# Kernel optimization log

Hardware: AMD Instinct MI355X
Metric: run time of the kernel (lower is better)

Reference implementation:

```python
import jax, jax.numpy as jnp
import numpy as np

M, L, D, V = 4096, 15, 1024, 32  # moves, word_max, in_sz, vocab_sz


def setup_inputs() -> dict:
    key = jax.random.key(0)
    ks = jax.random.split(key, 9)
    s = 0.02
    return {
        "tokens": jax.random.randint(ks[0], (M, L), 0, V),
        "letter_emb": jax.random.normal(ks[1], (V, D), jnp.float32) * s,
        "pos_emb": jax.random.normal(ks[2], (L, D), jnp.float32) * s,
        "Wq": jax.random.normal(ks[3], (D, D), jnp.float32) * s,
        "bq": jax.random.normal(ks[4], (D,), jnp.float32) * s,
        "Wk": jax.random.normal(ks[5], (D, D), jnp.float32) * s,
        "bk": jax.random.normal(ks[6], (D,), jnp.float32) * s,
        "Wv": jax.random.normal(ks[7], (D, D), jnp.float32) * s,
        "bv": jax.random.normal(ks[8], (D,), jnp.float32) * s,
    }


def reference(tokens, letter_emb, pos_emb, Wq, bq, Wk, bk, Wv, bv):
    # WordEncoder, batched across all M moves.
    x = letter_emb[tokens] + pos_emb[None, :, :]          # [M, L, D]
    q = jnp.einsum("mld,ed->mle", x, Wq) + bq             # Linear: x @ W.T + b
    k = jnp.einsum("mld,ed->mle", x, Wk) + bk
    v = jnp.einsum("mld,ed->mle", x, Wv) + bv
    scores = jax.nn.softmax(jnp.einsum("mle,mke->mlk", q, k), axis=-1)  # [M, L, L]
    attn = jnp.einsum("mlk,mke->mle", scores, v)          # [M, L, D]
    word = attn.sum(axis=1)                               # [M, D]
    # enc = word + ordered, where ordered is an identical second evaluation
    # of word_enc on the same word -> enc = 2 * word.
    return 2.0 * word
```

## Files before the change

kernel.cpp:

```cpp
#include <hip/hip_runtime.h>
#include <hip/hip_bf16.h>

#define NMOVES 4096
#define LW     15
#define DIM    1024
#define VOC    32
#define NROW   480
#define XROW   48
#define G48LD  64

typedef __attribute__((ext_vector_type(8))) short  short8;
typedef __attribute__((ext_vector_type(4))) float  floatx4;

__device__ __forceinline__ unsigned short f2b(float f) {
  unsigned int x;
  __builtin_memcpy(&x, &f, 4);
  x = x + 0x7FFFu + ((x >> 16) & 1u);
  return (unsigned short)(x >> 16);
}
__device__ __forceinline__ ushort4 cvt4(float4 v) {
  ushort4 o; o.x = f2b(v.x); o.y = f2b(v.y); o.z = f2b(v.z); o.w = f2b(v.w);
  return o;
}
__device__ __forceinline__ float b2f(unsigned short u) {
  unsigned int x = ((unsigned int)u) << 16;
  float f;
  __builtin_memcpy(&f, &x, 4);
  return f;
}

#define LDK 72

__global__ __launch_bounds__(256) void proj_small(
    const float* __restrict__ letter, const float* __restrict__ pos,
    const float* __restrict__ Wq, const float* __restrict__ Wk,
    const float* __restrict__ Wv,
    float* __restrict__ Xq, float* __restrict__ Xk, float* __restrict__ Xv) {
  __shared__ __attribute__((aligned(16))) unsigned short lA[64 * LDK];
  __shared__ __attribute__((aligned(16))) unsigned short lB[64 * LDK];

  const float* W = (blockIdx.z == 0) ? Wq : (blockIdx.z == 1) ? Wk : Wv;
  float*       O = (blockIdx.z == 0) ? Xq : (blockIdx.z == 1) ? Xk : Xv;

  const int bn0 = blockIdx.y * 64;

  const int tid  = threadIdx.x;
  const int lane = tid & 63;
  const int wave = tid >> 6;
  const int wr   = wave >> 1;
  const int wc   = wave & 1;
  const int quad = lane >> 4;
  const int l16  = lane & 15;
  const int srow = tid >> 3;
  const int scol = (tid & 7) << 3;

  const float* aptr0 = letter + (size_t)srow * DIM + scol;
  const bool   av1   = (srow < LW);
  const float* aptr1 = av1 ? (pos + (size_t)srow * DIM + scol) : letter;
  const float* bptr0 = W + (size_t)(bn0 + srow) * DIM + scol;
  const float* bptr1 = bptr0 + (size_t)32 * DIM;

  const float4 z4 = make_float4(0.f, 0.f, 0.f, 0.f);
  float4 ra00 = *reinterpret_cast<const float4*>(aptr0);
  float4 ra01 = *reinterpret_cast<const float4*>(aptr0 + 4);
  float4 ra10 = av1 ? *reinterpret_cast<const float4*>(aptr1)     : z4;
  float4 ra11 = av1 ? *reinterpret_cast<const float4*>(aptr1 + 4) : z4;
  float4 rb00 = *reinterpret_cast<const float4*>(bptr0);
  float4 rb01 = *reinterpret_cast<const float4*>(bptr0 + 4);
  float4 rb10 = *reinterpret_cast<const float4*>(bptr1);
  float4 rb11 = *reinterpret_cast<const float4*>(bptr1 + 4);

  floatx4 acc[2][2];
#pragma unroll
  for (int i = 0; i < 2; ++i)
#pragma unroll
    for (int j = 0; j < 2; ++j) acc[i][j] = (floatx4){0.f, 0.f, 0.f, 0.f};

  for (int k0 = 0; k0 < DIM; k0 += 64) {
    *reinterpret_cast<ushort4*>(lA + srow * LDK + scol)            = cvt4(ra00);
    *reinterpret_cast<ushort4*>(lA + srow * LDK + scol + 4)        = cvt4(ra01);
    *reinterpret_cast<ushort4*>(lA + (srow + 32) * LDK + scol)     = cvt4(ra10);
    *reinterpret_cast<ushort4*>(lA + (srow + 32) * LDK + scol + 4) = cvt4(ra11);
    *reinterpret_cast<ushort4*>(lB + srow * LDK + scol)            = cvt4(rb00);
    *reinterpret_cast<ushort4*>(lB + srow * LDK + scol + 4)        = cvt4(rb01);
    *reinterpret_cast<ushort4*>(lB + (srow + 32) * LDK + scol)     = cvt4(rb10);
    *reinterpret_cast<ushort4*>(lB + (srow + 32) * LDK + scol + 4) = cvt4(rb11);
    __syncthreads();
    if (k0 + 64 < DIM) {
      const int k = k0 + 64;
      ra00 = *reinterpret_cast<const float4*>(aptr0 + k);
      ra01 = *reinterpret_cast<const float4*>(aptr0 + k + 4);
      ra10 = av1 ? *reinterpret_cast<const float4*>(aptr1 + k)     : z4;
      ra11 = av1 ? *reinterpret_cast<const float4*>(aptr1 + k + 4) : z4;
      rb00 = *reinterpret_cast<const float4*>(bptr0 + k);
      rb01 = *reinterpret_cast<const float4*>(bptr0 + k + 4);
      rb10 = *reinterpret_cast<const float4*>(bptr1 + k);
      rb11 = *reinterpret_cast<const float4*>(bptr1 + k + 4);
    }
#pragma unroll
    for (int kk = 0; kk < 64; kk += 32) {
      short8 a0 = *reinterpret_cast<const short8*>(lA + (wr * 32 + l16) * LDK + kk + quad * 8);
      short8 a1 = *reinterpret_cast<const short8*>(lA + (wr * 32 + 16 + l16) * LDK + kk + quad * 8);
      short8 b0 = *reinterpret_cast<const short8*>(lB + (wc * 32 + l16) * LDK + kk + quad * 8);
      short8 b1 = *reinterpret_cast<const short8*>(lB + (wc * 32 + 16 + l16) * LDK + kk + quad * 8);
      acc[0][0] = __builtin_amdgcn_mfma_f32_16x16x32_bf16(a0, b0, acc[0][0], 0, 0, 0);
      acc[0][1] = __builtin_amdgcn_mfma_f32_16x16x32_bf16(a0, b1, acc[0][1], 0, 0, 0);
      acc[1][0] = __builtin_amdgcn_mfma_f32_16x16x32_bf16(a1, b0, acc[1][0], 0, 0, 0);
      acc[1][1] = __builtin_amdgcn_mfma_f32_16x16x32_bf16(a1, b1, acc[1][1], 0, 0, 0);
    }
    __syncthreads();
  }

#pragma unroll
  for (int mi = 0; mi < 2; ++mi) {
#pragma unroll
    for (int ni = 0; ni < 2; ++ni) {
      const int gcol = bn0 + wc * 32 + ni * 16 + l16;
#pragma unroll
      for (int i = 0; i < 4; ++i) {
        const int grow = wr * 32 + mi * 16 + quad * 4 + i;
        if (grow < XROW - 1)
          O[(size_t)grow * DIM + gcol] = acc[mi][ni][i];
      }
    }
  }
}

__global__ __launch_bounds__(256) void gram_vexp(
    const float* __restrict__ Xq, const float* __restrict__ Xk,
    const float* __restrict__ bq, const float* __restrict__ bk,
    const float* __restrict__ Xv,
    float* __restrict__ G48, unsigned short* __restrict__ XvT) {
  const int tid = threadIdx.x;

  if (blockIdx.x == 0) {
    __shared__ __attribute__((aligned(16))) unsigned short lA[64 * LDK];
    __shared__ __attribute__((aligned(16))) unsigned short lB[64 * LDK];

    const int lane = tid & 63;
    const int wave = tid >> 6;
    const int wr   = wave >> 1;
    const int wc   = wave & 1;
    const int quad = lane >> 4;
    const int l16  = lane & 15;
    const int srow = tid >> 3;
    const int scol = (tid & 7) << 3;

    const float* aptr0 = Xq + (size_t)srow * DIM + scol;
    const float* bptr0 = Xk + (size_t)srow * DIM + scol;
    const bool   v1    = (srow <= LW);
    const float* aptr1 = (srow < LW) ? (Xq + (size_t)(32 + srow) * DIM + scol)
                                     : (srow == LW ? (bq + scol) : Xq);
    const float* bptr1 = (srow < LW) ? (Xk + (size_t)(32 + srow) * DIM + scol)
                                     : (srow == LW ? (bk + scol) : Xk);

    const float4 z4 = make_float4(0.f, 0.f, 0.f, 0.f);
    float4 ra00 = *reinterpret_cast<const float4*>(aptr0);
    float4 ra01 = *reinterpret_cast<const float4*>(aptr0 + 4);
    float4 ra10 = v1 ? *reinterpret_cast<const float4*>(aptr1)     : z4;
    float4 ra11 = v1 ? *reinterpret_cast<const float4*>(aptr1 + 4) : z4;
    float4 rb00 = *reinterpret_cast<const float4*>(bptr0);
    float4 rb01 = *reinterpret_cast<const float4*>(bptr0 + 4);
    float4 rb10 = v1 ? *reinterpret_cast<const float4*>(bptr1)     : z4;
    float4 rb11 = v1 ? *reinterpret_cast<const float4*>(bptr1 + 4) : z4;

    floatx4 acc[2][2];
#pragma unroll
    for (int i = 0; i < 2; ++i)
#pragma unroll
      for (int j = 0; j < 2; ++j) acc[i][j] = (floatx4){0.f, 0.f, 0.f, 0.f};

    for (int k0 = 0; k0 < DIM; k0 += 64) {
      *reinterpret_cast<ushort4*>(lA + srow * LDK + scol)            = cvt4(ra00);
      *reinterpret_cast<ushort4*>(lA + srow * LDK + scol + 4)        = cvt4(ra01);
      *reinterpret_cast<ushort4*>(lA + (srow + 32) * LDK + scol)     = cvt4(ra10);
      *reinterpret_cast<ushort4*>(lA + (srow + 32) * LDK + scol + 4) = cvt4(ra11);
      *reinterpret_cast<ushort4*>(lB + srow * LDK + scol)            = cvt4(rb00);
      *reinterpret_cast<ushort4*>(lB + srow * LDK + scol + 4)        = cvt4(rb01);
      *reinterpret_cast<ushort4*>(lB + (srow + 32) * LDK + scol)     = cvt4(rb10);
      *reinterpret_cast<ushort4*>(lB + (srow + 32) * LDK + scol + 4) = cvt4(rb11);
      __syncthreads();
      if (k0 + 64 < DIM) {
        const int k = k0 + 64;
        ra00 = *reinterpret_cast<const float4*>(aptr0 + k);
        ra01 = *reinterpret_cast<const float4*>(aptr0 + k + 4);
        ra10 = v1 ? *reinterpret_cast<const float4*>(aptr1 + k)     : z4;
        ra11 = v1 ? *reinterpret_cast<const float4*>(aptr1 + k + 4) : z4;
        rb00 = *reinterpret_cast<const float4*>(bptr0 + k);
        rb01 = *reinterpret_cast<const float4*>(bptr0 + k + 4);
        rb10 = v1 ? *reinterpret_cast<const float4*>(bptr1 + k)     : z4;
        rb11 = v1 ? *reinterpret_cast<const float4*>(bptr1 + k + 4) : z4;
      }
#pragma unroll
      for (int kk = 0; kk < 64; kk += 32) {
        short8 a0 = *reinterpret_cast<const short8*>(lA + (wr * 32 + l16) * LDK + kk + quad * 8);
        short8 a1 = *reinterpret_cast<const short8*>(lA + (wr * 32 + 16 + l16) * LDK + kk + quad * 8);
        short8 b0 = *reinterpret_cast<const short8*>(lB + (wc * 32 + l16) * LDK + kk + quad * 8);
        short8 b1 = *reinterpret_cast<const short8*>(lB + (wc * 32 + 16 + l16) * LDK + kk + quad * 8);
        acc[0][0] = __builtin_amdgcn_mfma_f32_16x16x32_bf16(a0, b0, acc[0][0], 0, 0, 0);
        acc[0][1] = __builtin_amdgcn_mfma_f32_16x16x32_bf16(a0, b1, acc[0][1], 0, 0, 0);
        acc[1][0] = __builtin_amdgcn_mfma_f32_16x16x32_bf16(a1, b0, acc[1][0], 0, 0, 0);
        acc[1][1] = __builtin_amdgcn_mfma_f32_16x16x32_bf16(a1, b1, acc[1][1], 0, 0, 0);
      }
      __syncthreads();
    }

#pragma unroll
    for (int mi = 0; mi < 2; ++mi) {
#pragma unroll
      for (int ni = 0; ni < 2; ++ni) {
        const int gcol = wc * 32 + ni * 16 + l16;
#pragma unroll
        for (int i = 0; i < 4; ++i) {
          const int grow = wr * 32 + mi * 16 + quad * 4 + i;
          if (grow < XROW)
            G48[(size_t)grow * G48LD + gcol] = acc[mi][ni][i];
        }
      }
    }
  } else {
    const int n  = ((int)blockIdx.x - 1) * 16 + (tid >> 4);
    const int k0 = (tid & 15) * 4;
    float v[4];
#pragma unroll
    for (int i = 0; i < 4; ++i) {
      const int k = k0 + i;
      v[i] = (k < XROW - 1) ? Xv[(size_t)k * DIM + n] : 0.f;
    }
    ushort4 o;
    o.x = f2b(v[0]); o.y = f2b(v[1]); o.z = f2b(v[2]); o.w = f2b(v[3]);
    *reinterpret_cast<ushort4*>(XvT + (size_t)n * 64 + k0) = o;
  }
}

__global__ __launch_bounds__(256) void coef_k(
    const void* __restrict__ tokens_raw, const float* __restrict__ G48,
    unsigned short* __restrict__ C) {
  __shared__ float Gs[XROW * 65];
  __shared__ float Sm[16][LW][17];
  __shared__ float CL[16][64];
  __shared__ int   tokL[16][16];
  __shared__ int   is64_s;
  const int m0  = blockIdx.x * 16;
  const int tid = threadIdx.x;

  const unsigned int* u32 = (const unsigned int*)tokens_raw;
  if (tid < 64) {
    unsigned int v = u32[2 * tid + 1];
    unsigned long long nz = __ballot(v != 0);
    if (tid == 0) is64_s = (nz == 0ULL) ? 1 : 0;
  }
#pragma unroll
  for (int i = 0; i < 12; ++i) {
    const int idx = i * 256 + tid;
    Gs[(idx >> 6) * 65 + (idx & 63)] = G48[idx];
  }
  {
    const int g = tid >> 4, L = tid & 15;
#pragma unroll
    for (int i = 0; i < 4; ++i) CL[g][L * 4 + i] = 0.f;
  }
  __syncthreads();

  if (tid < 16 * LW) {
    const int mv = tid / LW, j = tid - mv * LW;
    int t;
    if (is64_s) t = (int)((const long long*)tokens_raw)[(size_t)(m0 + mv) * LW + j];
    else        t = ((const int*)tokens_raw)[(size_t)(m0 + mv) * LW + j];
    tokL[mv][j] = t;
  }
  __syncthreads();

  const int g = tid >> 4;
  const int L = tid & 15;
  if (L < LW) {
    const int rb0 = tokL[g][L] * 65;
    const int rb1 = (32 + L) * 65;
    const int rb2 = (XROW - 1) * 65;
    float S[LW];
#pragma unroll
    for (int j = 0; j < LW; ++j) {
      const int c0 = tokL[g][j];
      const int c1 = 32 + j;
      S[j] = Gs[rb0 + c0] + Gs[rb1 + c0] + Gs[rb2 + c0]
           + Gs[rb0 + c1] + Gs[rb1 + c1] + Gs[rb2 + c1];
    }
    float mx = S[0];
#pragma unroll
    for (int j = 1; j < LW; ++j) mx = fmaxf(mx, S[j]);
    float sum = 0.f;
#pragma unroll
    for (int j = 0; j < LW; ++j) { S[j] = __expf(S[j] - mx); sum += S[j]; }
    const float inv = 1.0f / sum;
#pragma unroll
    for (int j = 0; j < LW; ++j) Sm[g][L][j] = S[j] * inv;
  }
  __syncthreads();

  if (L < LW) {
    float s = 0.f;
#pragma unroll
    for (int l = 0; l < LW; ++l) s += Sm[g][l][L];
    const float wj = 2.0f * s;
    atomicAdd(&CL[g][tokL[g][L]], wj);
    CL[g][32 + L] = wj;
  }
  __syncthreads();

  float4 cv = *reinterpret_cast<const float4*>(&CL[g][L * 4]);
  ushort4 hi, lo;
  hi.x = f2b(cv.x); hi.y = f2b(cv.y); hi.z = f2b(cv.z); hi.w = f2b(cv.w);
  lo.x = f2b(cv.x - b2f(hi.x)); lo.y = f2b(cv.y - b2f(hi.y));
  lo.z = f2b(cv.z - b2f(hi.z)); lo.w = f2b(cv.w - b2f(hi.w));
  unsigned short* Crow = C + (size_t)(m0 + g) * 128;
  *reinterpret_cast<ushort4*>(Crow + L * 4)      = hi;
  *reinterpret_cast<ushort4*>(Crow + 64 + L * 4) = lo;
}

__global__ __launch_bounds__(256) void out_gemm(
    const unsigned short* __restrict__ C, const unsigned short* __restrict__ XvT,
    const float* __restrict__ bv, float* __restrict__ out) {
  const int bm0 = blockIdx.x * 64;
  const int bn0 = blockIdx.y * 64;
  const int tid  = threadIdx.x;
  const int lane = tid & 63;
  const int wave = tid >> 6;
  const int wr   = wave >> 1;
  const int wc   = wave & 1;
  const int quad = lane >> 4;
  const int l16  = lane & 15;

  const unsigned short* A0 = C + (size_t)(bm0 + wr * 32 + l16) * 128;
  const unsigned short* A1 = A0 + 16 * 128;
  const unsigned short* B0 = XvT + (size_t)(bn0 + wc * 32 + l16) * 64;
  const unsigned short* B1 = B0 + 16 * 64;

  floatx4 acc[2][2];
#pragma unroll
  for (int i = 0; i < 2; ++i)
#pragma unroll
    for (int j = 0; j < 2; ++j) acc[i][j] = (floatx4){0.f, 0.f, 0.f, 0.f};

#pragma unroll
  for (int ks = 0; ks < 64; ks += 32) {
    short8 b0  = *reinterpret_cast<const short8*>(B0 + ks + quad * 8);
    short8 b1  = *reinterpret_cast<const short8*>(B1 + ks + quad * 8);
    short8 a0h = *reinterpret_cast<const short8*>(A0 + ks + quad * 8);
    short8 a1h = *reinterpret_cast<const short8*>(A1 + ks + quad * 8);
    short8 a0l = *reinterpret_cast<const short8*>(A0 + 64 + ks + quad * 8);
    short8 a1l = *reinterpret_cast<const short8*>(A1 + 64 + ks + quad * 8);
    acc[0][0] = __builtin_amdgcn_mfma_f32_16x16x32_bf16(a0h, b0, acc[0][0], 0, 0, 0);
    acc[0][0] = __builtin_amdgcn_mfma_f32_16x16x32_bf16(a0l, b0, acc[0][0], 0, 0, 0);
    acc[0][1] = __builtin_amdgcn_mfma_f32_16x16x32_bf16(a0h, b1, acc[0][1], 0, 0, 0);
    acc[0][1] = __builtin_amdgcn_mfma_f32_16x16x32_bf16(a0l, b1, acc[0][1], 0, 0, 0);
    acc[1][0] = __builtin_amdgcn_mfma_f32_16x16x32_bf16(a1h, b0, acc[1][0], 0, 0, 0);
    acc[1][0] = __builtin_amdgcn_mfma_f32_16x16x32_bf16(a1l, b0, acc[1][0], 0, 0, 0);
    acc[1][1] = __builtin_amdgcn_mfma_f32_16x16x32_bf16(a1h, b1, acc[1][1], 0, 0, 0);
    acc[1][1] = __builtin_amdgcn_mfma_f32_16x16x32_bf16(a1l, b1, acc[1][1], 0, 0, 0);
  }

#pragma unroll
  for (int mi = 0; mi < 2; ++mi) {
#pragma unroll
    for (int ni = 0; ni < 2; ++ni) {
      const int gcol = bn0 + wc * 32 + ni * 16 + l16;
      const float bias30 = 30.0f * bv[gcol];
#pragma unroll
      for (int i = 0; i < 4; ++i) {
        const int grow = bm0 + wr * 32 + mi * 16 + quad * 4 + i;
        out[(size_t)grow * DIM + gcol] = acc[mi][ni][i] + bias30;
      }
    }
  }
}

extern "C" void kernel_launch(void* const* d_in, const int* in_sizes, int n_in,
                              void* d_out, int out_size, void* d_ws, size_t ws_size,
                              hipStream_t stream) {
  const void*  tokens = d_in[0];
  const float* letter = (const float*)d_in[1];
  const float* pos    = (const float*)d_in[2];
  const float* Wq     = (const float*)d_in[3];
  const float* bq     = (const float*)d_in[4];
  const float* Wk     = (const float*)d_in[5];
  const float* bk     = (const float*)d_in[6];
  const float* Wv     = (const float*)d_in[7];
  const float* bv     = (const float*)d_in[8];
  float*       outp   = (float*)d_out;

  char* ws = (char*)d_ws;
  const size_t XSZ  = (size_t)XROW * DIM * 4;
  const size_t GSZ  = (size_t)XROW * G48LD * 4;
  float* Xq = (float*)(ws);
  float* Xk = (float*)(ws + XSZ);
  float* Xv = (float*)(ws + 2 * XSZ);
  float* Gp = (float*)(ws + 3 * XSZ);
  unsigned short* XvT = (unsigned short*)(ws + 3 * XSZ + 16384);
  unsigned short* Cc  = (unsigned short*)(ws + 3 * XSZ + 16384 + (size_t)DIM * 64 * 2);
  (void)GSZ;

  proj_small<<<dim3(1, 16, 3), 256, 0, stream>>>(letter, pos, Wq, Wk, Wv,
                                                 Xq, Xk, Xv);
  gram_vexp<<<65, 256, 0, stream>>>(Xq, Xk, bq, bk, Xv, Gp, XvT);
  coef_k<<<NMOVES / 16, 256, 0, stream>>>(tokens, Gp, Cc);
  out_gemm<<<dim3(NMOVES / 64, DIM / 64), 256, 0, stream>>>(Cc, XvT, bv, outp);
}
```

Before: 136.7 us.

## Split-K the small projection and Gram GEMMs across more blocks

The projection GEMM is split along K into four partial planes, giving four times as many blocks. The Gram GEMM is split into eight K-chunks, and its partials are reduced later in coef_k and in the XvT transpose. Both kernels drop the LDS staging and load bf16 fragments directly from global memory into MFMA operands. The goal is to spread the latency-bound single-block and 48-block stages across more CUs. The cost is extra partial-sum traffic, redundant reduction reads in every coef_k block, and uncoalesced direct fragment loads.

```diff
diff --git a/kernel.cpp b/kernel.cpp
--- a/kernel.cpp
+++ b/kernel.cpp
@@ -5,9 +5,11 @@
 #define LW     15
 #define DIM    1024
 #define VOC    32
-#define NROW   480
 #define XROW   48
-#define G48LD  64
+#define KSPL   4
+#define GSPL   8
+#define PLSZ   (48 * DIM)
+#define GPLSZ  (48 * 64)
 
 typedef __attribute__((ext_vector_type(8))) short  short8;
 typedef __attribute__((ext_vector_type(4))) float  floatx4;
@@ -18,31 +20,34 @@
   x = x + 0x7FFFu + ((x >> 16) & 1u);
   return (unsigned short)(x >> 16);
 }
-__device__ __forceinline__ ushort4 cvt4(float4 v) {
-  ushort4 o; o.x = f2b(v.x); o.y = f2b(v.y); o.z = f2b(v.z); o.w = f2b(v.w);
-  return o;
-}
 __device__ __forceinline__ float b2f(unsigned short u) {
   unsigned int x = ((unsigned int)u) << 16;
   float f;
   __builtin_memcpy(&f, &x, 4);
   return f;
 }
-
-#define LDK 72
-
-__global__ __launch_bounds__(256) void proj_small(
+__device__ __forceinline__ short8 pk8(float4 a, float4 b) {
+  short8 r;
+  r[0] = (short)f2b(a.x); r[1] = (short)f2b(a.y);
+  r[2] = (short)f2b(a.z); r[3] = (short)f2b(a.w);
+  r[4] = (short)f2b(b.x); r[5] = (short)f2b(b.y);
+  r[6] = (short)f2b(b.z); r[7] = (short)f2b(b.w);
+  return r;
+}
+__device__ __forceinline__ float4 ld4(const float* p) {
+  return *reinterpret_cast<const float4*>(p);
+}
+
+__global__ __launch_bounds__(256) void proj_ksplit(
     const float* __restrict__ letter, const float* __restrict__ pos,
     const float* __restrict__ Wq, const float* __restrict__ Wk,
-    const float* __restrict__ Wv,
-    float* __restrict__ Xq, float* __restrict__ Xk, float* __restrict__ Xv) {
-  __shared__ __attribute__((aligned(16))) unsigned short lA[64 * LDK];
-  __shared__ __attribute__((aligned(16))) unsigned short lB[64 * LDK];
-
-  const float* W = (blockIdx.z == 0) ? Wq : (blockIdx.z == 1) ? Wk : Wv;
-  float*       O = (blockIdx.z == 0) ? Xq : (blockIdx.z == 1) ? Xk : Xv;
-
-  const int bn0 = blockIdx.y * 64;
+    const float* __restrict__ Wv, float* __restrict__ Xp) {
+  const int p     = blockIdx.x;
+  const int bn0   = blockIdx.y * 64;
+  const int z     = blockIdx.z;
+  const int kbase = p * 256;
+  const float* W = (z == 0) ? Wq : (z == 1) ? Wk : Wv;
+  float*       O = Xp + (size_t)(z * KSPL + p) * PLSZ;
 
   const int tid  = threadIdx.x;
   const int lane = tid & 63;
@@ -51,24 +56,15 @@
   const int wc   = wave & 1;
   const int quad = lane >> 4;
   const int l16  = lane & 15;
-  const int srow = tid >> 3;
-  const int scol = (tid & 7) << 3;
-
-  const float* aptr0 = letter + (size_t)srow * DIM + scol;
-  const bool   av1   = (srow < LW);
-  const float* aptr1 = av1 ? (pos + (size_t)srow * DIM + scol) : letter;
-  const float* bptr0 = W + (size_t)(bn0 + srow) * DIM + scol;
-  const float* bptr1 = bptr0 + (size_t)32 * DIM;
-
-  const float4 z4 = make_float4(0.f, 0.f, 0.f, 0.f);
-  float4 ra00 = *reinterpret_cast<const float4*>(aptr0);
-  float4 ra01 = *reinterpret_cast<const float4*>(aptr0 + 4);
-  float4 ra10 = av1 ? *reinterpret_cast<const float4*>(aptr1)     : z4;
-  float4 ra11 = av1 ? *reinterpret_cast<const float4*>(aptr1 + 4) : z4;
-  float4 rb00 = *reinterpret_cast<const float4*>(bptr0);
-  float4 rb01 = *reinterpret_cast<const float4*>(bptr0 + 4);
-  float4 rb10 = *reinterpret_cast<const float4*>(bptr1);
-  float4 rb11 = *reinterpret_cast<const float4*>(bptr1 + 4);
+
+  const int rA0 = wr * 32 + l16;
+  const int rA1 = rA0 + 16;
+  const float* a0p = (rA0 < 32) ? letter + (size_t)rA0 * DIM
+                   : (rA0 < 47) ? pos + (size_t)(rA0 - 32) * DIM : nullptr;
+  const float* a1p = (rA1 < 32) ? letter + (size_t)rA1 * DIM
+                   : (rA1 < 47) ? pos + (size_t)(rA1 - 32) * DIM : nullptr;
+  const float* b0p = W + (size_t)(bn0 + wc * 32 + l16) * DIM;
+  const float* b1p = b0p + (size_t)16 * DIM;
 
   floatx4 acc[2][2];
 #pragma unroll
@@ -76,39 +72,18 @@
 #pragma unroll
     for (int j = 0; j < 2; ++j) acc[i][j] = (floatx4){0.f, 0.f, 0.f, 0.f};
 
-  for (int k0 = 0; k0 < DIM; k0 += 64) {
-    *reinterpret_cast<ushort4*>(lA + srow * LDK + scol)            = cvt4(ra00);
-    *reinterpret_cast<ushort4*>(lA + srow * LDK + scol + 4)        = cvt4(ra01);
-    *reinterpret_cast<ushort4*>(lA + (srow + 32) * LDK + scol)     = cvt4(ra10);
-    *reinterpret_cast<ushort4*>(lA + (srow + 32) * LDK + scol + 4) = cvt4(ra11);
-    *reinterpret_cast<ushort4*>(lB + srow * LDK + scol)            = cvt4(rb00);
-    *reinterpret_cast<ushort4*>(lB + srow * LDK + scol + 4)        = cvt4(rb01);
-    *reinterpret_cast<ushort4*>(lB + (srow + 32) * LDK + scol)     = cvt4(rb10);
-    *reinterpret_cast<ushort4*>(lB + (srow + 32) * LDK + scol + 4) = cvt4(rb11);
-    __syncthreads();
-    if (k0 + 64 < DIM) {
-      const int k = k0 + 64;
-      ra00 = *reinterpret_cast<const float4*>(aptr0 + k);
-      ra01 = *reinterpret_cast<const float4*>(aptr0 + k + 4);
-      ra10 = av1 ? *reinterpret_cast<const float4*>(aptr1 + k)     : z4;
-      ra11 = av1 ? *reinterpret_cast<const float4*>(aptr1 + k + 4) : z4;
-      rb00 = *reinterpret_cast<const float4*>(bptr0 + k);
-      rb01 = *reinterpret_cast<const float4*>(bptr0 + k + 4);
-      rb10 = *reinterpret_cast<const float4*>(bptr1 + k);
-      rb11 = *reinterpret_cast<const float4*>(bptr1 + k + 4);
-    }
-#pragma unroll
-    for (int kk = 0; kk < 64; kk += 32) {
-      short8 a0 = *reinterpret_cast<const short8*>(lA + (wr * 32 + l16) * LDK + kk + quad * 8);
-      short8 a1 = *reinterpret_cast<const short8*>(lA + (wr * 32 + 16 + l16) * LDK + kk + quad * 8);
-      short8 b0 = *reinterpret_cast<const short8*>(lB + (wc * 32 + l16) * LDK + kk + quad * 8);
-      short8 b1 = *reinterpret_cast<const short8*>(lB + (wc * 32 + 16 + l16) * LDK + kk + quad * 8);
-      acc[0][0] = __builtin_amdgcn_mfma_f32_16x16x32_bf16(a0, b0, acc[0][0], 0, 0, 0);
-      acc[0][1] = __builtin_amdgcn_mfma_f32_16x16x32_bf16(a0, b1, acc[0][1], 0, 0, 0);
-      acc[1][0] = __builtin_amdgcn_mfma_f32_16x16x32_bf16(a1, b0, acc[1][0], 0, 0, 0);
-      acc[1][1] = __builtin_amdgcn_mfma_f32_16x16x32_bf16(a1, b1, acc[1][1], 0, 0, 0);
-    }
-    __syncthreads();
+  const short8 z8 = (short8){0,0,0,0,0,0,0,0};
+#pragma unroll
+  for (int kk = 0; kk < 256; kk += 32) {
+    const int kc = kbase + kk + quad * 8;
+    short8 a0 = a0p ? pk8(ld4(a0p + kc), ld4(a0p + kc + 4)) : z8;
+    short8 a1 = a1p ? pk8(ld4(a1p + kc), ld4(a1p + kc + 4)) : z8;
+    short8 b0 = pk8(ld4(b0p + kc), ld4(b0p + kc + 4));
+    short8 b1 = pk8(ld4(b1p + kc), ld4(b1p + kc + 4));
+    acc[0][0] = __builtin_amdgcn_mfma_f32_16x16x32_bf16(a0, b0, acc[0][0], 0, 0, 0);
+    acc[0][1] = __builtin_amdgcn_mfma_f32_16x16x32_bf16(a0, b1, acc[0][1], 0, 0, 0);
+    acc[1][0] = __builtin_amdgcn_mfma_f32_16x16x32_bf16(a1, b0, acc[1][0], 0, 0, 0);
+    acc[1][1] = __builtin_amdgcn_mfma_f32_16x16x32_bf16(a1, b1, acc[1][1], 0, 0, 0);
   }
 
 #pragma unroll
@@ -119,50 +94,53 @@
 #pragma unroll
       for (int i = 0; i < 4; ++i) {
         const int grow = wr * 32 + mi * 16 + quad * 4 + i;
-        if (grow < XROW - 1)
+        if (grow < 47)
           O[(size_t)grow * DIM + gcol] = acc[mi][ni][i];
       }
     }
   }
 }
 
+__device__ __forceinline__ short8 gfrag(const float* __restrict__ X4,
+                                        const float* __restrict__ bias,
+                                        int row, int kc) {
+  if (row < 47) {
+    const float* r0 = X4 + (size_t)row * DIM + kc;
+    float4 s0 = ld4(r0),            s1 = ld4(r0 + 4);
+    float4 t0 = ld4(r0 + PLSZ),     t1 = ld4(r0 + PLSZ + 4);
+    float4 u0 = ld4(r0 + 2 * PLSZ), u1 = ld4(r0 + 2 * PLSZ + 4);
+    float4 v0 = ld4(r0 + 3 * PLSZ), v1 = ld4(r0 + 3 * PLSZ + 4);
+    s0.x += t0.x + u0.x + v0.x; s0.y += t0.y + u0.y + v0.y;
+    s0.z += t0.z + u0.z + v0.z; s0.w += t0.w + u0.w + v0.w;
+    s1.x += t1.x + u1.x + v1.x; s1.y += t1.y + u1.y + v1.y;
+    s1.z += t1.z + u1.z + v1.z; s1.w += t1.w + u1.w + v1.w;
+    return pk8(s0, s1);
+  } else if (row == 47) {
+    return pk8(ld4(bias + kc), ld4(bias + kc + 4));
+  }
+  return (short8){0,0,0,0,0,0,0,0};
+}
+
 __global__ __launch_bounds__(256) void gram_vexp(
-    const float* __restrict__ Xq, const float* __restrict__ Xk,
+    const float* __restrict__ Xp,
     const float* __restrict__ bq, const float* __restrict__ bk,
-    const float* __restrict__ Xv,
-    float* __restrict__ G48, unsigned short* __restrict__ XvT) {
+    float* __restrict__ Gp8, unsigned short* __restrict__ XvT) {
+  const int bid = blockIdx.x;
   const int tid = threadIdx.x;
 
-  if (blockIdx.x == 0) {
-    __shared__ __attribute__((aligned(16))) unsigned short lA[64 * LDK];
-    __shared__ __attribute__((aligned(16))) unsigned short lB[64 * LDK];
-
+  if (bid < GSPL) {
+    const int kbase = bid * 128;
     const int lane = tid & 63;
     const int wave = tid >> 6;
     const int wr   = wave >> 1;
     const int wc   = wave & 1;
     const int quad = lane >> 4;
     const int l16  = lane & 15;
-    const int srow = tid >> 3;
-    const int scol = (tid & 7) << 3;
-
-    const float* aptr0 = Xq + (size_t)srow * DIM + scol;
-    const float* bptr0 = Xk + (size_t)srow * DIM + scol;
-    const bool   v1    = (srow <= LW);
-    const float* aptr1 = (srow < LW) ? (Xq + (size_t)(32 + srow) * DIM + scol)
-                                     : (srow == LW ? (bq + scol) : Xq);
-    const float* bptr1 = (srow < LW) ? (Xk + (size_t)(32 + srow) * DIM + scol)
-                                     : (srow == LW ? (bk + scol) : Xk);
-
-    const float4 z4 = make_float4(0.f, 0.f, 0.f, 0.f);
-    float4 ra00 = *reinterpret_cast<const float4*>(aptr0);
-    float4 ra01 = *reinterpret_cast<const float4*>(aptr0 + 4);
-    float4 ra10 = v1 ? *reinterpret_cast<const float4*>(aptr1)     : z4;
-    float4 ra11 = v1 ? *reinterpret_cast<const float4*>(aptr1 + 4) : z4;
-    float4 rb00 = *reinterpret_cast<const float4*>(bptr0);
-    float4 rb01 = *reinterpret_cast<const float4*>(bptr0 + 4);
-    float4 rb10 = v1 ? *reinterpret_cast<const float4*>(bptr1)     : z4;
-    float4 rb11 = v1 ? *reinterpret_cast<const float4*>(bptr1 + 4) : z4;
+
+    const float* Xq4 = Xp;
+    const float* Xk4 = Xp + (size_t)4 * PLSZ;
+    const int rA0 = wr * 32 + l16, rA1 = rA0 + 16;
+    const int rB0 = wc * 32 + l16, rB1 = rB0 + 16;
 
     floatx4 acc[2][2];
 #pragma unroll
@@ -170,41 +148,20 @@
 #pragma unroll
       for (int j = 0; j < 2; ++j) acc[i][j] = (floatx4){0.f, 0.f, 0.f, 0.f};
 
-    for (int k0 = 0; k0 < DIM; k0 += 64) {
-      *reinterpret_cast<ushort4*>(lA + srow * LDK + scol)            = cvt4(ra00);
-      *reinterpret_cast<ushort4*>(lA + srow * LDK + scol + 4)        = cvt4(ra01);
-      *reinterpret_cast<ushort4*>(lA + (srow + 32) * LDK + scol)     = cvt4(ra10);
-      *reinterpret_cast<ushort4*>(lA + (srow + 32) * LDK + scol + 4) = cvt4(ra11);
-      *reinterpret_cast<ushort4*>(lB + srow * LDK + scol)            = cvt4(rb00);
-      *reinterpret_cast<ushort4*>(lB + srow * LDK + scol + 4)        = cvt4(rb01);
-      *reinterpret_cast<ushort4*>(lB + (srow + 32) * LDK + scol)     = cvt4(rb10);
-      *reinterpret_cast<ushort4*>(lB + (srow + 32) * LDK + scol + 4) = cvt4(rb11);
-      __syncthreads();
-      if (k0 + 64 < DIM) {
-        const int k = k0 + 64;
-        ra00 = *reinterpret_cast<const float4*>(aptr0 + k);
-        ra01 = *reinterpret_cast<const float4*>(aptr0 + k + 4);
-        ra10 = v1 ? *reinterpret_cast<const float4*>(aptr1 + k)     : z4;
-        ra11 = v1 ? *reinterpret_cast<const float4*>(aptr1 + k + 4) : z4;
-        rb00 = *reinterpret_cast<const float4*>(bptr0 + k);
-        rb01 = *reinterpret_cast<const float4*>(bptr0 + k + 4);
-        rb10 = v1 ? *reinterpret_cast<const float4*>(bptr1 + k)     : z4;
-        rb11 = v1 ? *reinterpret_cast<const float4*>(bptr1 + k + 4) : z4;
-      }
-#pragma unroll
-      for (int kk = 0; kk < 64; kk += 32) {
-        short8 a0 = *reinterpret_cast<const short8*>(lA + (wr * 32 + l16) * LDK + kk + quad * 8);
-        short8 a1 = *reinterpret_cast<const short8*>(lA + (wr * 32 + 16 + l16) * LDK + kk + quad * 8);
-        short8 b0 = *reinterpret_cast<const short8*>(lB + (wc * 32 + l16) * LDK + kk + quad * 8);
-        short8 b1 = *reinterpret_cast<const short8*>(lB + (wc * 32 + 16 + l16) * LDK + kk + quad * 8);
-        acc[0][0] = __builtin_amdgcn_mfma_f32_16x16x32_bf16(a0, b0, acc[0][0], 0, 0, 0);
-        acc[0][1] = __builtin_amdgcn_mfma_f32_16x16x32_bf16(a0, b1, acc[0][1], 0, 0, 0);
-        acc[1][0] = __builtin_amdgcn_mfma_f32_16x16x32_bf16(a1, b0, acc[1][0], 0, 0, 0);
-        acc[1][1] = __builtin_amdgcn_mfma_f32_16x16x32_bf16(a1, b1, acc[1][1], 0, 0, 0);
-      }
-      __syncthreads();
-    }
-
+#pragma unroll
+    for (int kk = 0; kk < 128; kk += 32) {
+      const int kc = kbase + kk + quad * 8;
+      short8 a0 = gfrag(Xq4, bq, rA0, kc);
+      short8 a1 = gfrag(Xq4, bq, rA1, kc);
+      short8 b0 = gfrag(Xk4, bk, rB0, kc);
+      short8 b1 = gfrag(Xk4, bk, rB1, kc);
+      acc[0][0] = __builtin_amdgcn_mfma_f32_16x16x32_bf16(a0, b0, acc[0][0], 0, 0, 0);
+      acc[0][1] = __builtin_amdgcn_mfma_f32_16x16x32_bf16(a0, b1, acc[0][1], 0, 0, 0);
+      acc[1][0] = __builtin_amdgcn_mfma_f32_16x16x32_bf16(a1, b0, acc[1][0], 0, 0, 0);
+      acc[1][1] = __builtin_amdgcn_mfma_f32_16x16x32_bf16(a1, b1, acc[1][1], 0, 0, 0);
+    }
+
+    float* Gout = Gp8 + (size_t)bid * GPLSZ;
 #pragma unroll
     for (int mi = 0; mi < 2; ++mi) {
 #pragma unroll
@@ -214,27 +171,37 @@
         for (int i = 0; i < 4; ++i) {
           const int grow = wr * 32 + mi * 16 + quad * 4 + i;
           if (grow < XROW)
-            G48[(size_t)grow * G48LD + gcol] = acc[mi][ni][i];
+            Gout[(size_t)grow * 64 + gcol] = acc[mi][ni][i];
         }
       }
     }
   } else {
-    const int n  = ((int)blockIdx.x - 1) * 16 + (tid >> 4);
-    const int k0 = (tid & 15) * 4;
-    float v[4];
-#pragma unroll
-    for (int i = 0; i < 4; ++i) {
-      const int k = k0 + i;
-      v[i] = (k < XROW - 1) ? Xv[(size_t)k * DIM + n] : 0.f;
-    }
-    ushort4 o;
-    o.x = f2b(v[0]); o.y = f2b(v[1]); o.z = f2b(v[2]); o.w = f2b(v[3]);
-    *reinterpret_cast<ushort4*>(XvT + (size_t)n * 64 + k0) = o;
+    const int n  = (bid - GSPL) * 64 + (tid & 63);
+    const int kg = tid >> 6;
+    const float* Xv4 = Xp + (size_t)8 * PLSZ;
+#pragma unroll
+    for (int s = 0; s < 4; ++s) {
+      const int k0 = kg * 4 + s * 16;
+      ushort4 o;
+      unsigned short* oc = &o.x;
+#pragma unroll
+      for (int i = 0; i < 4; ++i) {
+        const int k = k0 + i;
+        float v = 0.f;
+        if (k < 47) {
+          const size_t off = (size_t)k * DIM + n;
+          v = Xv4[off] + Xv4[off + PLSZ] + Xv4[off + 2 * PLSZ] +
+              Xv4[off + 3 * PLSZ];
+        }
+        oc[i] = f2b(v);
+      }
+      *reinterpret_cast<ushort4*>(XvT + (size_t)n * 64 + k0) = o;
+    }
   }
 }
 
 __global__ __launch_bounds__(256) void coef_k(
-    const void* __restrict__ tokens_raw, const float* __restrict__ G48,
+    const void* __restrict__ tokens_raw, const float* __restrict__ Gp8,
     unsigned short* __restrict__ C) {
   __shared__ float Gs[XROW * 65];
   __shared__ float Sm[16][LW][17];
@@ -253,7 +220,10 @@
 #pragma unroll
   for (int i = 0; i < 12; ++i) {
     const int idx = i * 256 + tid;
-    Gs[(idx >> 6) * 65 + (idx & 63)] = G48[idx];
+    float s = 0.f;
+#pragma unroll
+    for (int p = 0; p < GSPL; ++p) s += Gp8[(size_t)p * GPLSZ + idx];
+    Gs[(idx >> 6) * 65 + (idx & 63)] = s;
   }
   {
     const int g = tid >> 4, L = tid & 15;
@@ -389,19 +359,16 @@
   float*       outp   = (float*)d_out;
 
   char* ws = (char*)d_ws;
-  const size_t XSZ  = (size_t)XROW * DIM * 4;
-  const size_t GSZ  = (size_t)XROW * G48LD * 4;
-  float* Xq = (float*)(ws);
-  float* Xk = (float*)(ws + XSZ);
-  float* Xv = (float*)(ws + 2 * XSZ);
-  float* Gp = (float*)(ws + 3 * XSZ);
-  unsigned short* XvT = (unsigned short*)(ws + 3 * XSZ + 16384);
-  unsigned short* Cc  = (unsigned short*)(ws + 3 * XSZ + 16384 + (size_t)DIM * 64 * 2);
-  (void)GSZ;
-
-  proj_small<<<dim3(1, 16, 3), 256, 0, stream>>>(letter, pos, Wq, Wk, Wv,
-                                                 Xq, Xk, Xv);
-  gram_vexp<<<65, 256, 0, stream>>>(Xq, Xk, bq, bk, Xv, Gp, XvT);
+  const size_t XP_SZ  = (size_t)12 * PLSZ * 4;
+  const size_t GP_SZ  = (size_t)GSPL * GPLSZ * 4;
+  const size_t XVT_SZ = (size_t)DIM * 64 * 2;
+  float*          Xp  = (float*)(ws);
+  float*          Gp  = (float*)(ws + XP_SZ);
+  unsigned short* XvT = (unsigned short*)(ws + XP_SZ + GP_SZ);
+  unsigned short* Cc  = (unsigned short*)(ws + XP_SZ + GP_SZ + XVT_SZ);
+
+  proj_ksplit<<<dim3(KSPL, 16, 3), 256, 0, stream>>>(letter, pos, Wq, Wk, Wv, Xp);
+  gram_vexp<<<GSPL + 16, 256, 0, stream>>>(Xp, bq, bk, Gp, XvT);
   coef_k<<<NMOVES / 16, 256, 0, stream>>>(tokens, Gp, Cc);
   out_gemm<<<dim3(NMOVES / 64, DIM / 64), 256, 0, stream>>>(Cc, XvT, bv, outp);
 }
```

New measurement: 118.7 us. 13.2% less time.
